# Optimization experiments

Hardware: AMD Instinct MI355X
Metric: run time of the kernel (lower is better)

The kernel has to match this reference:

```python
import jax, jax.numpy as jnp
import numpy as np

N = 100000      # nodes
E = 1600000     # edges
G = 1024        # graphs in batch
NF = 9          # atom features (OGB AtomEncoder)
V = 128         # vocab per atom feature
H = 128         # hidden_dim
L = 3           # num_graph_layers
OUT = 10        # output_dim
BN_EPS = 1e-5


def setup_inputs() -> dict:
    key = jax.random.key(0)
    ks = jax.random.split(key, 12)
    x = jax.random.randint(ks[0], (N, NF), 0, V, dtype=jnp.int32)
    edge_index = jax.random.randint(ks[1], (2, E), 0, N, dtype=jnp.int32)
    batch = jnp.sort(jax.random.randint(ks[2], (N,), 0, G, dtype=jnp.int32))
    emb = jax.random.normal(ks[3], (NF, V, H), dtype=jnp.float32) * 0.05
    Ws = jax.random.normal(ks[4], (L, H, H), dtype=jnp.float32) * (1.0 / np.sqrt(H))
    bs = jnp.zeros((L, H), dtype=jnp.float32)
    gamma = jnp.ones((L - 1, H), dtype=jnp.float32)
    beta = jnp.zeros((L - 1, H), dtype=jnp.float32)
    run_mean = jax.random.normal(ks[5], (L - 1, H), dtype=jnp.float32) * 0.1
    run_var = jax.random.uniform(ks[6], (L - 1, H), minval=0.5, maxval=1.5, dtype=jnp.float32)
    W_clf = jax.random.normal(ks[7], (H, OUT), dtype=jnp.float32) * (1.0 / np.sqrt(H))
    b_clf = jnp.zeros((OUT,), dtype=jnp.float32)
    return {"x": x, "edge_index": edge_index, "batch": batch, "emb": emb,
            "Ws": Ws, "bs": bs, "gamma": gamma, "beta": beta,
            "run_mean": run_mean, "run_var": run_var,
            "W_clf": W_clf, "b_clf": b_clf}


def reference(x, edge_index, batch, emb, Ws, bs, gamma, beta, run_mean, run_var, W_clf, b_clf):
    # Eval-mode forward: dropout = identity, BatchNorm uses running stats.
    src, dst = edge_index[0], edge_index[1]
    # GCN symmetric normalization with self-loops: deg = 1 + in-degree
    deg = jax.ops.segment_sum(jnp.ones((E,), jnp.float32), dst, num_segments=N) + 1.0
    dinv = jax.lax.rsqrt(deg)                 # [N]
    norm_e = dinv[src] * dinv[dst]            # [E] edge coefficient
    norm_self = dinv * dinv                   # [N] self-loop coefficient

    # AtomEncoder: sum of per-feature embedding lookups -> [N, H]
    h = emb[jnp.arange(NF)[None, :], x].sum(axis=1)

    for i in range(L):
        hw = h @ Ws[i]                                                       # [N, H]
        h = (jax.ops.segment_sum(hw[src] * norm_e[:, None], dst, num_segments=N)
             + hw * norm_self[:, None] + bs[i])                              # GCNConv
        if i < L - 1:
            h = (h - run_mean[i]) * (gamma[i] * jax.lax.rsqrt(run_var[i] + BN_EPS)) + beta[i]
            h = jax.nn.relu(h)

    # global mean pool over graphs
    counts = jax.ops.segment_sum(jnp.ones((N,), jnp.float32), batch, num_segments=G)
    pooled = jax.ops.segment_sum(h, batch, num_segments=G) / jnp.maximum(counts, 1.0)[:, None]
    return pooled @ W_clf + b_clf             # [G, OUT]
```

## Files before the change

kernel.cpp:

```cpp
#include <hip/hip_runtime.h>
#include <hip/hip_bf16.h>
#include <hip/hip_fp16.h>

#define NN 100000
#define EE 1600000
#define GG 1024
#define NF 9
#define VV 128
#define HH 128
#define LL 3
#define OUTD 10
#define BN_EPS 1e-5f
#define NBUCK 196
#define BCAP 12288
#define CHUNK 4096
#define NB128 782

typedef __attribute__((ext_vector_type(8))) short short8;
typedef __attribute__((ext_vector_type(4))) float f32x4;

__device__ inline unsigned short f2bf(float x) {
    unsigned u = __float_as_uint(x);
    unsigned r = (u + 0x7fffu + ((u >> 16) & 1u)) >> 16;
    return (unsigned short)r;
}
__device__ inline float bf2f(unsigned short b) { return __uint_as_float(((unsigned)b) << 16); }

__device__ inline void mix8(float a[8], const uint4& r, float nm) {
    asm("v_fma_mix_f32 %0, %8, %12, %0 op_sel:[0,0,0] op_sel_hi:[1,0,0]\n\t"
        "v_fma_mix_f32 %1, %8, %12, %1 op_sel:[1,0,0] op_sel_hi:[1,0,0]\n\t"
        "v_fma_mix_f32 %2, %9, %12, %2 op_sel:[0,0,0] op_sel_hi:[1,0,0]\n\t"
        "v_fma_mix_f32 %3, %9, %12, %3 op_sel:[1,0,0] op_sel_hi:[1,0,0]\n\t"
        "v_fma_mix_f32 %4, %10, %12, %4 op_sel:[0,0,0] op_sel_hi:[1,0,0]\n\t"
        "v_fma_mix_f32 %5, %10, %12, %5 op_sel:[1,0,0] op_sel_hi:[1,0,0]\n\t"
        "v_fma_mix_f32 %6, %11, %12, %6 op_sel:[0,0,0] op_sel_hi:[1,0,0]\n\t"
        "v_fma_mix_f32 %7, %11, %12, %7 op_sel:[1,0,0] op_sel_hi:[1,0,0]"
        : "+v"(a[0]), "+v"(a[1]), "+v"(a[2]), "+v"(a[3]),
          "+v"(a[4]), "+v"(a[5]), "+v"(a[6]), "+v"(a[7])
        : "v"(r.x), "v"(r.y), "v"(r.z), "v"(r.w), "v"(nm));
}

__global__ __launch_bounds__(256) void split_kernel(const int* __restrict__ src,
                                                    const int* __restrict__ dst,
                                                    int* __restrict__ bcur,
                                                    int* __restrict__ bucket_edges) {
    __shared__ int lcnt[256], loff[256], lcur[256], gbase[256], sh[256];
    __shared__ int stage[CHUNK];
    __shared__ unsigned char stageb[CHUNK];
    int tid = threadIdx.x;
    int cs = blockIdx.x * CHUNK;
    int n = min(CHUNK, EE - cs);
    lcnt[tid] = 0;
    __syncthreads();
    for (int i = tid; i < n; i += 256)
        atomicAdd(&lcnt[dst[cs + i] >> 9], 1);
    __syncthreads();
    int val = lcnt[tid];
    sh[tid] = val; __syncthreads();
    for (int d = 1; d < 256; d <<= 1) {
        int t = (tid >= d) ? sh[tid - d] : 0;
        __syncthreads();
        sh[tid] += t;
        __syncthreads();
    }
    loff[tid] = sh[tid] - val;
    lcur[tid] = sh[tid] - val;
    __syncthreads();
    for (int i = tid; i < n; i += 256) {
        int d = dst[cs + i], s = src[cs + i];
        int b = d >> 9;
        int p = atomicAdd(&lcur[b], 1);
        stage[p] = (s << 9) | (d & 511);
        stageb[p] = (unsigned char)b;
    }
    if (val > 0) gbase[tid] = atomicAdd(&bcur[tid], val);
    __syncthreads();
    for (int i = tid; i < n; i += 256) {
        int b = stageb[i];
        bucket_edges[(size_t)b * BCAP + gbase[b] + (i - loff[b])] = stage[i];
    }
}

__global__ __launch_bounds__(256) void bhist_kernel(const int* __restrict__ bcur,
                                                    const int* __restrict__ bucket_edges,
                                                    int* __restrict__ cnt,
                                                    float* __restrict__ dinv,
                                                    int* __restrict__ bsum) {
    __shared__ int lc[512];
    __shared__ int sh[256];
    int b = blockIdx.x, tid = threadIdx.x;
    lc[tid] = 0; lc[tid + 256] = 0;
    __syncthreads();
    int n = bcur[b];
    const int* be = bucket_edges + (size_t)b * BCAP;
    for (int i = tid; i < n; i += 256) atomicAdd(&lc[be[i] & 511], 1);
    __syncthreads();
    int node = b * 512 + tid;
    int c0 = lc[tid], c1 = lc[tid + 256];
    int s = 0;
    if (node < NN) { cnt[node] = c0; dinv[node] = rsqrtf(1.0f + (float)c0); s += c0; }
    if (node + 256 < NN) { cnt[node + 256] = c1; dinv[node + 256] = rsqrtf(1.0f + (float)c1); s += c1; }
    sh[tid] = s; __syncthreads();
    for (int d = 128; d > 0; d >>= 1) { if (tid < d) sh[tid] += sh[tid + d]; __syncthreads(); }
    if (tid == 0) bsum[b] = sh[0];
}

__global__ void scanB_kernel(int* __restrict__ bsum) {
    __shared__ int sh[256];
    int tid = threadIdx.x;
    int v = (tid < NBUCK) ? bsum[tid] : 0;
    sh[tid] = v; __syncthreads();
    for (int d = 1; d < 256; d <<= 1) {
        int t = (tid >= d) ? sh[tid - d] : 0;
        __syncthreads();
        sh[tid] += t;
        __syncthreads();
    }
    if (tid < NBUCK) bsum[tid] = sh[tid] - v;
}

__global__ void scanC_kernel(const int* __restrict__ cnt, const int* __restrict__ bsum,
                             int* __restrict__ row_ptr) {
    __shared__ int sh[256];
    int tid = threadIdx.x;
    int base = blockIdx.x * 512 + tid * 2;
    int v0 = (base < NN) ? cnt[base] : 0;
    int v1 = (base + 1 < NN) ? cnt[base + 1] : 0;
    int ts = v0 + v1;
    sh[tid] = ts; __syncthreads();
    for (int d = 1; d < 256; d <<= 1) {
        int t = (tid >= d) ? sh[tid - d] : 0;
        __syncthreads();
        sh[tid] += t;
        __syncthreads();
    }
    int excl = sh[tid] - ts + bsum[blockIdx.x];
    if (base < NN) row_ptr[base] = excl;
    if (base + 1 < NN) row_ptr[base + 1] = excl + v0;
    if (blockIdx.x == 0 && tid == 0) row_ptr[NN] = EE;
}

__global__ __launch_bounds__(256) void cscatter_kernel(const int* __restrict__ bcur,
                                                       const int* __restrict__ bucket_edges,
                                                       const int* __restrict__ row_ptr,
                                                       const float* __restrict__ dinv,
                                                       int2* __restrict__ col) {
    __shared__ int lcur[512];
    int b = blockIdx.x, tid = threadIdx.x;
    int node0 = b * 512;
#pragma unroll
    for (int k = 0; k < 2; ++k) {
        int j = tid + k * 256;
        int node = node0 + j;
        if (node < NN) lcur[j] = row_ptr[node];
    }
    __syncthreads();
    int n = bcur[b];
    const int* be = bucket_edges + (size_t)b * BCAP;
    for (int i = tid; i < n; i += 256) {
        int w = be[i];
        int j = w & 511;
        int s = (int)((unsigned)w >> 9);
        int p = atomicAdd(&lcur[j], 1);
        float nm = dinv[s] * dinv[node0 + j];
        col[p] = make_int2(s, __float_as_int(nm));
    }
}

__global__ __launch_bounds__(256) void wprep_kernel(const float* __restrict__ Ws,
        const float* __restrict__ Wc, const float* __restrict__ b2,
        unsigned short* __restrict__ WThi, unsigned short* __restrict__ WTlo,
        unsigned short* __restrict__ WcThi, unsigned short* __restrict__ WcTlo,
        float* __restrict__ bb2) {
    int id = blockIdx.x * 256 + threadIdx.x;
    if (id < LL * HH * HH) {
        int layer = id >> 14;
        int rem = id & (HH * HH - 1);
        int k = rem >> 7, n = rem & 127;
        float w = Ws[id];
        unsigned short hi = f2bf(w);
        float lo = w - bf2f(hi);
        WThi[(size_t)layer * HH * HH + n * HH + k] = hi;
        WTlo[(size_t)layer * HH * HH + n * HH + k] = f2bf(lo);
    }
    if (blockIdx.x == 0) {
        int tid = threadIdx.x;
        const float* W2 = Ws + (size_t)2 * HH * HH;
        for (int i = tid; i < 16 * HH; i += 256) {
            int n = i >> 7, k = i & 127;
            float s = 0.f;
            if (n < OUTD) {
                for (int j = 0; j < HH; ++j)
                    s += W2[k * HH + j] * Wc[j * OUTD + n];
            }
            unsigned short hi = f2bf(s);
            WcThi[i] = hi;
            WcTlo[i] = f2bf(s - bf2f(hi));
        }
        if (tid < OUTD) {
            float s = 0.f;
            for (int c = 0; c < HH; ++c) s += b2[c] * Wc[c * OUTD + tid];
            bb2[tid] = s;
        }
    }
}

__global__ __launch_bounds__(256) void enc_mm_kernel(const int* __restrict__ x,
        const float* __restrict__ emb,
        const unsigned short* __restrict__ WThi, const unsigned short* __restrict__ WTlo,
        __half* __restrict__ hw_out) {
    __shared__ __align__(16) unsigned short lh[32][136];
    __shared__ __align__(16) unsigned short ll[32][136];
    int tid = threadIdx.x;
    int nloc = tid >> 3;
    int seg = tid & 7;
    int nodebase = blockIdx.x * 32;
    int n = nodebase + nloc;
    float s[16];
#pragma unroll
    for (int i = 0; i < 16; ++i) s[i] = 0.f;
#pragma unroll
    for (int f = 0; f < NF; ++f) {
        int idx = x[n * NF + f];
        const float4* ep = (const float4*)(emb + ((size_t)(f * VV + idx)) * HH + seg * 16);
#pragma unroll
        for (int q = 0; q < 4; ++q) {
            float4 e = ep[q];
            s[q * 4 + 0] += e.x; s[q * 4 + 1] += e.y;
            s[q * 4 + 2] += e.z; s[q * 4 + 3] += e.w;
        }
    }
#pragma unroll
    for (int q = 0; q < 4; ++q) {
        ushort4 oh, ol;
        oh.x = f2bf(s[q * 4 + 0]); ol.x = f2bf(s[q * 4 + 0] - bf2f(oh.x));
        oh.y = f2bf(s[q * 4 + 1]); ol.y = f2bf(s[q * 4 + 1] - bf2f(oh.y));
        oh.z = f2bf(s[q * 4 + 2]); ol.z = f2bf(s[q * 4 + 2] - bf2f(oh.z));
        oh.w = f2bf(s[q * 4 + 3]); ol.w = f2bf(s[q * 4 + 3] - bf2f(oh.w));
        *(ushort4*)&lh[nloc][seg * 16 + q * 4] = oh;
        *(ushort4*)&ll[nloc][seg * 16 + q * 4] = ol;
    }
    __syncthreads();
    int wave = tid >> 6, lane = tid & 63;
    int quad = lane >> 4, m = lane & 15;
    f32x4 acc[2][2] = {};
    int kq = quad * 8;
#pragma unroll
    for (int t = 0; t < 4; ++t) {
        int k0 = t * 32 + kq;
        short8 a0h = *(const short8*)&lh[m][k0];
        short8 a0l = *(const short8*)&ll[m][k0];
        short8 a1h = *(const short8*)&lh[16 + m][k0];
        short8 a1l = *(const short8*)&ll[16 + m][k0];
#pragma unroll
        for (int c = 0; c < 2; ++c) {
            int ct = wave * 2 + c;
            short8 bh = *(const short8*)(WThi + (size_t)(ct * 16 + m) * HH + k0);
            short8 bl = *(const short8*)(WTlo + (size_t)(ct * 16 + m) * HH + k0);
            acc[0][c] = __builtin_amdgcn_mfma_f32_16x16x32_bf16(a0h, bh, acc[0][c], 0, 0, 0);
            acc[0][c] = __builtin_amdgcn_mfma_f32_16x16x32_bf16(a0l, bh, acc[0][c], 0, 0, 0);
            acc[0][c] = __builtin_amdgcn_mfma_f32_16x16x32_bf16(a0h, bl, acc[0][c], 0, 0, 0);
            acc[1][c] = __builtin_amdgcn_mfma_f32_16x16x32_bf16(a1h, bh, acc[1][c], 0, 0, 0);
            acc[1][c] = __builtin_amdgcn_mfma_f32_16x16x32_bf16(a1l, bh, acc[1][c], 0, 0, 0);
            acc[1][c] = __builtin_amdgcn_mfma_f32_16x16x32_bf16(a1h, bl, acc[1][c], 0, 0, 0);
        }
    }
#pragma unroll
    for (int c = 0; c < 2; ++c) {
        int colx = (wave * 2 + c) * 16 + m;
#pragma unroll
        for (int rt = 0; rt < 2; ++rt) {
            int r0 = nodebase + rt * 16 + quad * 4;
#pragma unroll
            for (int reg = 0; reg < 4; ++reg)
                hw_out[(size_t)(r0 + reg) * HH + colx] = __float2half(acc[rt][c][reg]);
        }
    }
}

__device__ inline void gather_node(const uint4* __restrict__ hw4,
                                   const int2* __restrict__ col,
                                   int start, int end, int c4,
                                   float a[8], float b[8]) {
    int e = start;
    for (; e + 4 <= end; e += 4) {
        unsigned long long w0 = *(const unsigned long long*)&col[e];
        unsigned long long w1 = *(const unsigned long long*)&col[e + 1];
        unsigned long long w2 = *(const unsigned long long*)&col[e + 2];
        unsigned long long w3 = *(const unsigned long long*)&col[e + 3];
        uint4 r0 = hw4[(size_t)(unsigned)(w0 & 0xffffffffu) * 16 + c4];
        uint4 r1 = hw4[(size_t)(unsigned)(w1 & 0xffffffffu) * 16 + c4];
        uint4 r2 = hw4[(size_t)(unsigned)(w2 & 0xffffffffu) * 16 + c4];
        uint4 r3 = hw4[(size_t)(unsigned)(w3 & 0xffffffffu) * 16 + c4];
        mix8(a, r0, __int_as_float((int)(unsigned)(w0 >> 32)));
        mix8(b, r1, __int_as_float((int)(unsigned)(w1 >> 32)));
        mix8(a, r2, __int_as_float((int)(unsigned)(w2 >> 32)));
        mix8(b, r3, __int_as_float((int)(unsigned)(w3 >> 32)));
    }
    if (e < end) {
        int last = end - 1;
        int e1 = min(e + 1, last), e2 = min(e + 2, last), e3 = min(e + 3, last);
        unsigned long long w0 = *(const unsigned long long*)&col[e];
        unsigned long long w1 = *(const unsigned long long*)&col[e1];
        unsigned long long w2 = *(const unsigned long long*)&col[e2];
        unsigned long long w3 = *(const unsigned long long*)&col[e3];
        float n0 = __int_as_float((int)(unsigned)(w0 >> 32));
        float n1 = (e + 1 < end) ? __int_as_float((int)(unsigned)(w1 >> 32)) : 0.f;
        float n2 = (e + 2 < end) ? __int_as_float((int)(unsigned)(w2 >> 32)) : 0.f;
        float n3 = (e + 3 < end) ? __int_as_float((int)(unsigned)(w3 >> 32)) : 0.f;
        uint4 r0 = hw4[(size_t)(unsigned)(w0 & 0xffffffffu) * 16 + c4];
        uint4 r1 = hw4[(size_t)(unsigned)(w1 & 0xffffffffu) * 16 + c4];
        uint4 r2 = hw4[(size_t)(unsigned)(w2 & 0xffffffffu) * 16 + c4];
        uint4 r3 = hw4[(size_t)(unsigned)(w3 & 0xffffffffu) * 16 + c4];
        mix8(a, r0, n0);
        mix8(b, r1, n1);
        mix8(a, r2, n2);
        mix8(b, r3, n3);
    }
}

template<bool DO_PROJ>
__global__ __launch_bounds__(512) void agg_mm_kernel(const __half* __restrict__ hw_in,
    const int* __restrict__ row_ptr, const int2* __restrict__ col,
    const float* __restrict__ dinv,
    const float* __restrict__ bias, const float* __restrict__ gamma,
    const float* __restrict__ beta, const float* __restrict__ rmean,
    const float* __restrict__ rvar,
    const unsigned short* __restrict__ WThi, const unsigned short* __restrict__ WTlo,
    __half* __restrict__ hw_out,
    const unsigned short* __restrict__ WcThi, const unsigned short* __restrict__ WcTlo,
    __half* __restrict__ y_out) {
    __shared__ __align__(16) unsigned short lh[32][136];
    __shared__ __align__(16) unsigned short ll[32][136];
    int wave = threadIdx.x >> 6;
    int lane = threadIdx.x & 63;
    int grp = lane >> 4;
    int c4 = lane & 15;
    int nodebase = blockIdx.x * 32;
    const uint4* hw4 = (const uint4*)hw_in;

    int v = nodebase + wave * 4 + grp;
    int start = row_ptr[v], end = row_ptr[v + 1];
    float a[8] = {}, b[8] = {};
    gather_node(hw4, col, start, end, c4, a, b);

    {
        float dv = dinv[v];
        uint4 r = hw4[(size_t)v * 16 + c4];
        mix8(a, r, dv * dv);
    }
#pragma unroll
    for (int i = 0; i < 8; ++i) a[i] += b[i];

    int ch = c4 * 8;
#pragma unroll
    for (int i = 0; i < 8; ++i) a[i] += bias[ch + i];
#pragma unroll
    for (int i = 0; i < 8; ++i) {
        int c = ch + i;
        float sc = gamma[c] * rsqrtf(rvar[c] + BN_EPS);
        a[i] = fmaxf((a[i] - rmean[c]) * sc + beta[c], 0.f);
    }
    int rloc = wave * 4 + grp;
    ushort4 oh0, oh1, ol0, ol1;
    oh0.x = f2bf(a[0]); ol0.x = f2bf(a[0] - bf2f(oh0.x));
    oh0.y = f2bf(a[1]); ol0.y = f2bf(a[1] - bf2f(oh0.y));
    oh0.z = f2bf(a[2]); ol0.z = f2bf(a[2] - bf2f(oh0.z));
    oh0.w = f2bf(a[3]); ol0.w = f2bf(a[3] - bf2f(oh0.w));
    oh1.x = f2bf(a[4]); ol1.x = f2bf(a[4] - bf2f(oh1.x));
    oh1.y = f2bf(a[5]); ol1.y = f2bf(a[5] - bf2f(oh1.y));
    oh1.z = f2bf(a[6]); ol1.z = f2bf(a[6] - bf2f(oh1.z));
    oh1.w = f2bf(a[7]); ol1.w = f2bf(a[7] - bf2f(oh1.w));
    *(ushort4*)&lh[rloc][ch]     = oh0;
    *(ushort4*)&lh[rloc][ch + 4] = oh1;
    *(ushort4*)&ll[rloc][ch]     = ol0;
    *(ushort4*)&ll[rloc][ch + 4] = ol1;

    __syncthreads();
    int quad = lane >> 4, m = lane & 15;
    f32x4 acc[2] = {};
    int kq = quad * 8;
    int ct = wave;
#pragma unroll
    for (int t = 0; t < 4; ++t) {
        int k0 = t * 32 + kq;
        short8 a0h = *(const short8*)&lh[m][k0];
        short8 a0l = *(const short8*)&ll[m][k0];
        short8 a1h = *(const short8*)&lh[16 + m][k0];
        short8 a1l = *(const short8*)&ll[16 + m][k0];
        short8 bh = *(const short8*)(WThi + (size_t)(ct * 16 + m) * HH + k0);
        short8 bl = *(const short8*)(WTlo + (size_t)(ct * 16 + m) * HH + k0);
        acc[0] = __builtin_amdgcn_mfma_f32_16x16x32_bf16(a0h, bh, acc[0], 0, 0, 0);
        acc[0] = __builtin_amdgcn_mfma_f32_16x16x32_bf16(a0l, bh, acc[0], 0, 0, 0);
        acc[0] = __builtin_amdgcn_mfma_f32_16x16x32_bf16(a0h, bl, acc[0], 0, 0, 0);
        acc[1] = __builtin_amdgcn_mfma_f32_16x16x32_bf16(a1h, bh, acc[1], 0, 0, 0);
        acc[1] = __builtin_amdgcn_mfma_f32_16x16x32_bf16(a1l, bh, acc[1], 0, 0, 0);
        acc[1] = __builtin_amdgcn_mfma_f32_16x16x32_bf16(a1h, bl, acc[1], 0, 0, 0);
    }
    int colx = ct * 16 + m;
#pragma unroll
    for (int rt = 0; rt < 2; ++rt) {
        int r0 = nodebase + rt * 16 + quad * 4;
#pragma unroll
        for (int reg = 0; reg < 4; ++reg)
            hw_out[(size_t)(r0 + reg) * HH + colx] = __float2half(acc[rt][reg]);
    }

    if constexpr (DO_PROJ) {
        if (wave < 2) {
            f32x4 pacc = {};
#pragma unroll
            for (int t = 0; t < 4; ++t) {
                int k0 = t * 32 + kq;
                short8 ah = *(const short8*)&lh[wave * 16 + m][k0];
                short8 al = *(const short8*)&ll[wave * 16 + m][k0];
                short8 bh = *(const short8*)(WcThi + (size_t)m * HH + k0);
                short8 bl = *(const short8*)(WcTlo + (size_t)m * HH + k0);
                pacc = __builtin_amdgcn_mfma_f32_16x16x32_bf16(ah, bh, pacc, 0, 0, 0);
                pacc = __builtin_amdgcn_mfma_f32_16x16x32_bf16(al, bh, pacc, 0, 0, 0);
                pacc = __builtin_amdgcn_mfma_f32_16x16x32_bf16(ah, bl, pacc, 0, 0, 0);
            }
#pragma unroll
            for (int reg = 0; reg < 4; ++reg) {
                int node = nodebase + wave * 16 + quad * 4 + reg;
                y_out[(size_t)node * 16 + m] = __float2half(pacc[reg]);
            }
        }
    }
}

__global__ __launch_bounds__(256) void agg_pool_kernel(const __half* __restrict__ y,
    const int* __restrict__ row_ptr, const int2* __restrict__ col,
    const float* __restrict__ dinv, const int* __restrict__ batch,
    float* __restrict__ pooled) {
    __shared__ __align__(16) float lz[128][16];
    __shared__ int bg[128];
    int tid = threadIdx.x;
    int g2 = tid >> 1;
    int cl = tid & 1;
    int nodebase = blockIdx.x * 128;
    int v = nodebase + g2;
    int vc = min(v, NN - 1);
    int start = row_ptr[vc];
    int end = (v < NN) ? row_ptr[vc + 1] : start;
    const uint4* y4 = (const uint4*)y;
    float a[8] = {};
    int e = start;
    for (; e + 4 <= end; e += 4) {
        unsigned long long w0 = *(const unsigned long long*)&col[e];
        unsigned long long w1 = *(const unsigned long long*)&col[e + 1];
        unsigned long long w2 = *(const unsigned long long*)&col[e + 2];
        unsigned long long w3 = *(const unsigned long long*)&col[e + 3];
        uint4 r0 = y4[(size_t)(unsigned)(w0 & 0xffffffffu) * 2 + cl];
        uint4 r1 = y4[(size_t)(unsigned)(w1 & 0xffffffffu) * 2 + cl];
        uint4 r2 = y4[(size_t)(unsigned)(w2 & 0xffffffffu) * 2 + cl];
        uint4 r3 = y4[(size_t)(unsigned)(w3 & 0xffffffffu) * 2 + cl];
        mix8(a, r0, __int_as_float((int)(unsigned)(w0 >> 32)));
        mix8(a, r1, __int_as_float((int)(unsigned)(w1 >> 32)));
        mix8(a, r2, __int_as_float((int)(unsigned)(w2 >> 32)));
        mix8(a, r3, __int_as_float((int)(unsigned)(w3 >> 32)));
    }
    if (e < end) {
        int last = end - 1;
        int e1 = min(e + 1, last), e2 = min(e + 2, last), e3 = min(e + 3, last);
        unsigned long long w0 = *(const unsigned long long*)&col[e];
        unsigned long long w1 = *(const unsigned long long*)&col[e1];
        unsigned long long w2 = *(const unsigned long long*)&col[e2];
        unsigned long long w3 = *(const unsigned long long*)&col[e3];
        float n0 = __int_as_float((int)(unsigned)(w0 >> 32));
        float n1 = (e + 1 < end) ? __int_as_float((int)(unsigned)(w1 >> 32)) : 0.f;
        float n2 = (e + 2 < end) ? __int_as_float((int)(unsigned)(w2 >> 32)) : 0.f;
        float n3 = (e + 3 < end) ? __int_as_float((int)(unsigned)(w3 >> 32)) : 0.f;
        uint4 r0 = y4[(size_t)(unsigned)(w0 & 0xffffffffu) * 2 + cl];
        uint4 r1 = y4[(size_t)(unsigned)(w1 & 0xffffffffu) * 2 + cl];
        uint4 r2 = y4[(size_t)(unsigned)(w2 & 0xffffffffu) * 2 + cl];
        uint4 r3 = y4[(size_t)(unsigned)(w3 & 0xffffffffu) * 2 + cl];
        mix8(a, r0, n0);
        mix8(a, r1, n1);
        mix8(a, r2, n2);
        mix8(a, r3, n3);
    }
    if (v < NN) {
        float dv = dinv[v];
        uint4 r = y4[(size_t)v * 2 + cl];
        mix8(a, r, dv * dv);
    } else {
#pragma unroll
        for (int i = 0; i < 8; ++i) a[i] = 0.f;
    }
    int chb = cl * 8;
#pragma unroll
    for (int i = 0; i < 8; ++i) lz[g2][chb + i] = a[i];
    if (cl == 0) bg[g2] = batch[vc];
    __syncthreads();
    int ch = tid & 15;
    int rh = tid >> 4;
    int r0i = rh * 8;
    int curg = bg[r0i];
    float run = 0.f;
    for (int r = r0i; r < r0i + 8; ++r) {
        int gg = bg[r];
        if (gg != curg) {
            atomicAdd(&pooled[(size_t)curg * 16 + ch], run);
            run = 0.f; curg = gg;
        }
        run += lz[r][ch];
    }
    atomicAdd(&pooled[(size_t)curg * 16 + ch], run);
}

__global__ __launch_bounds__(256) void finalize_kernel(const float* __restrict__ pooled,
    const int* __restrict__ batch, const float* __restrict__ bb2,
    const float* __restrict__ bc, float* __restrict__ out) {
    int id = blockIdx.x * 256 + threadIdx.x;
    if (id >= GG * 16) return;
    int g = id >> 4, o = id & 15;
    if (o >= OUTD) return;
    int lo = 0, hi = NN;
    while (lo < hi) { int mid = (lo + hi) >> 1; if (batch[mid] < g) lo = mid + 1; else hi = mid; }
    int s0 = lo;
    lo = 0; hi = NN;
    int g1 = g + 1;
    while (lo < hi) { int mid = (lo + hi) >> 1; if (batch[mid] < g1) lo = mid + 1; else hi = mid; }
    int cnt = lo - s0;
    float r = pooled[(size_t)g * 16 + o] / fmaxf((float)cnt, 1.0f);
    out[(size_t)g * OUTD + o] = r + ((cnt > 0) ? bb2[o] : 0.f) + bc[o];
}

extern "C" void kernel_launch(void* const* d_in, const int* in_sizes, int n_in,
                              void* d_out, int out_size, void* d_ws, size_t ws_size,
                              hipStream_t stream) {
    const int*   x      = (const int*)d_in[0];
    const int*   eidx   = (const int*)d_in[1];
    const int*   batch  = (const int*)d_in[2];
    const float* emb    = (const float*)d_in[3];
    const float* Ws     = (const float*)d_in[4];
    const float* bs     = (const float*)d_in[5];
    const float* gamma  = (const float*)d_in[6];
    const float* beta   = (const float*)d_in[7];
    const float* rmean  = (const float*)d_in[8];
    const float* rvar   = (const float*)d_in[9];
    const float* Wclf   = (const float*)d_in[10];
    const float* bclf   = (const float*)d_in[11];
    float* out = (float*)d_out;

    const int* e_src = eidx;
    const int* e_dst = eidx + EE;

    char* ws = (char*)d_ws;
    size_t off = 0;
    auto take = [&](size_t bytes) -> void* {
        void* p = ws + off;
        off = (off + bytes + 255) & ~(size_t)255;
        return p;
    };
    float* dinv     = (float*)take((size_t)NN * 4);
    int*   cnt      = (int*)  take((size_t)NN * 4);
    int*   row_ptr  = (int*)  take((size_t)(NN + 1) * 4);
    int*   bsum     = (int*)  take((size_t)NBUCK * 4);
    int*   bcur     = (int*)  take((size_t)256 * 4);
    int*   bucket_edges = (int*)take((size_t)NBUCK * BCAP * 4);
    int2*  col      = (int2*) take((size_t)EE * 8 + 64);
    __half* hwA     = (__half*)take((size_t)NN * HH * 2);
    __half* hwB     = (__half*)take((size_t)NN * HH * 2);
    __half* yh      = (__half*)take((size_t)NN * 16 * 2);
    float* pooled   = (float*)take((size_t)GG * 16 * 4);
    unsigned short* WThi = (unsigned short*)take((size_t)LL * HH * HH * 2);
    unsigned short* WTlo = (unsigned short*)take((size_t)LL * HH * HH * 2);
    unsigned short* WcThi = (unsigned short*)take((size_t)16 * HH * 2);
    unsigned short* WcTlo = (unsigned short*)take((size_t)16 * HH * 2);
    float* bb2      = (float*)take((size_t)16 * 4);

    hipMemsetAsync(bcur, 0, 256 * 4, stream);
    hipMemsetAsync(pooled, 0, (size_t)GG * 16 * 4, stream);

    split_kernel<<<(EE + CHUNK - 1) / CHUNK, 256, 0, stream>>>(e_src, e_dst, bcur, bucket_edges);
    bhist_kernel<<<NBUCK, 256, 0, stream>>>(bcur, bucket_edges, cnt, dinv, bsum);
    scanB_kernel<<<1, 256, 0, stream>>>(bsum);
    scanC_kernel<<<NBUCK, 256, 0, stream>>>(cnt, bsum, row_ptr);
    cscatter_kernel<<<NBUCK, 256, 0, stream>>>(bcur, bucket_edges, row_ptr, dinv, col);
    wprep_kernel<<<(LL * HH * HH + 255) / 256, 256, 0, stream>>>(Ws, Wclf, bs + 2 * HH,
        WThi, WTlo, WcThi, WcTlo, bb2);

    enc_mm_kernel<<<NN / 32, 256, 0, stream>>>(x, emb, WThi, WTlo, hwA);
    agg_mm_kernel<false><<<NN / 32, 512, 0, stream>>>(hwA, row_ptr, col, dinv,
        bs, gamma, beta, rmean, rvar,
        WThi + (size_t)1 * HH * HH, WTlo + (size_t)1 * HH * HH, hwB,
        nullptr, nullptr, nullptr);
    agg_mm_kernel<true><<<NN / 32, 512, 0, stream>>>(hwB, row_ptr, col, dinv,
        bs + HH, gamma + HH, beta + HH, rmean + HH, rvar + HH,
        WThi + (size_t)2 * HH * HH, WTlo + (size_t)2 * HH * HH, hwA,
        WcThi, WcTlo, yh);
    agg_pool_kernel<<<NB128, 256, 0, stream>>>(yh, row_ptr, col, dinv, batch, pooled);
    finalize_kernel<<<(GG * 16 + 255) / 256, 256, 0, stream>>>(pooled, batch, bb2, bclf, out);
}
```

Before: 411.2 us.

## Replace bucketed CSR build with global-atomic histogram and direct placement

```diff
diff --git a/kernel.cpp b/kernel.cpp
--- a/kernel.cpp
+++ b/kernel.cpp
@@ -11,9 +11,7 @@
 #define LL 3
 #define OUTD 10
 #define BN_EPS 1e-5f
-#define NBUCK 196
-#define BCAP 12288
-#define CHUNK 4096
+#define NB_SCAN 98
 #define NB128 782
 
 typedef __attribute__((ext_vector_type(8))) short short8;
@@ -40,129 +38,75 @@
         : "v"(r.x), "v"(r.y), "v"(r.z), "v"(r.w), "v"(nm));
 }
 
-__global__ __launch_bounds__(256) void split_kernel(const int* __restrict__ src,
-                                                    const int* __restrict__ dst,
-                                                    int* __restrict__ bcur,
-                                                    int* __restrict__ bucket_edges) {
-    __shared__ int lcnt[256], loff[256], lcur[256], gbase[256], sh[256];
-    __shared__ int stage[CHUNK];
-    __shared__ unsigned char stageb[CHUNK];
+__global__ __launch_bounds__(256) void hist_kernel(const int* __restrict__ dst,
+                                                   int* __restrict__ cnt) {
+    int i = blockIdx.x * 256 + threadIdx.x;
+    int stride = gridDim.x * 256;
+    for (; i < EE; i += stride) atomicAdd(&cnt[dst[i]], 1);
+}
+
+__global__ void scanA_kernel(const int* __restrict__ cnt, int* __restrict__ bsum,
+                             float* __restrict__ dinv) {
+    __shared__ int sh[256];
     int tid = threadIdx.x;
-    int cs = blockIdx.x * CHUNK;
-    int n = min(CHUNK, EE - cs);
-    lcnt[tid] = 0;
+    int base = blockIdx.x * 1024 + tid * 4;
+    int s = 0;
+#pragma unroll
+    for (int i = 0; i < 4; ++i) {
+        int idx = base + i;
+        if (idx < NN) {
+            int c = cnt[idx];
+            s += c;
+            dinv[idx] = rsqrtf(1.0f + (float)c);
+        }
+    }
+    sh[tid] = s; __syncthreads();
+    for (int d = 128; d > 0; d >>= 1) { if (tid < d) sh[tid] += sh[tid + d]; __syncthreads(); }
+    if (tid == 0) bsum[blockIdx.x] = sh[0];
+}
+
+__global__ void scanC_kernel(const int* __restrict__ cnt, const int* __restrict__ bsum,
+                             int* __restrict__ row_ptr, int* __restrict__ cur) {
+    __shared__ int sh[256];
+    __shared__ int pre[256];
+    int tid = threadIdx.x;
+    pre[tid] = (tid < blockIdx.x) ? bsum[tid] : 0;
     __syncthreads();
-    for (int i = tid; i < n; i += 256)
-        atomicAdd(&lcnt[dst[cs + i] >> 9], 1);
-    __syncthreads();
-    int val = lcnt[tid];
-    sh[tid] = val; __syncthreads();
+    for (int d = 128; d > 0; d >>= 1) { if (tid < d) pre[tid] += pre[tid + d]; __syncthreads(); }
+    int bbase = pre[0];
+    int base = blockIdx.x * 1024 + tid * 4;
+    int v[4];
+#pragma unroll
+    for (int i = 0; i < 4; ++i) { int idx = base + i; v[i] = (idx < NN) ? cnt[idx] : 0; }
+    int tsum = v[0] + v[1] + v[2] + v[3];
+    sh[tid] = tsum; __syncthreads();
     for (int d = 1; d < 256; d <<= 1) {
         int t = (tid >= d) ? sh[tid - d] : 0;
         __syncthreads();
         sh[tid] += t;
         __syncthreads();
     }
-    loff[tid] = sh[tid] - val;
-    lcur[tid] = sh[tid] - val;
-    __syncthreads();
-    for (int i = tid; i < n; i += 256) {
-        int d = dst[cs + i], s = src[cs + i];
-        int b = d >> 9;
-        int p = atomicAdd(&lcur[b], 1);
-        stage[p] = (s << 9) | (d & 511);
-        stageb[p] = (unsigned char)b;
-    }
-    if (val > 0) gbase[tid] = atomicAdd(&bcur[tid], val);
-    __syncthreads();
-    for (int i = tid; i < n; i += 256) {
-        int b = stageb[i];
-        bucket_edges[(size_t)b * BCAP + gbase[b] + (i - loff[b])] = stage[i];
-    }
-}
-
-__global__ __launch_bounds__(256) void bhist_kernel(const int* __restrict__ bcur,
-                                                    const int* __restrict__ bucket_edges,
-                                                    int* __restrict__ cnt,
-                                                    float* __restrict__ dinv,
-                                                    int* __restrict__ bsum) {
-    __shared__ int lc[512];
-    __shared__ int sh[256];
-    int b = blockIdx.x, tid = threadIdx.x;
-    lc[tid] = 0; lc[tid + 256] = 0;
-    __syncthreads();
-    int n = bcur[b];
-    const int* be = bucket_edges + (size_t)b * BCAP;
-    for (int i = tid; i < n; i += 256) atomicAdd(&lc[be[i] & 511], 1);
-    __syncthreads();
-    int node = b * 512 + tid;
-    int c0 = lc[tid], c1 = lc[tid + 256];
-    int s = 0;
-    if (node < NN) { cnt[node] = c0; dinv[node] = rsqrtf(1.0f + (float)c0); s += c0; }
-    if (node + 256 < NN) { cnt[node + 256] = c1; dinv[node + 256] = rsqrtf(1.0f + (float)c1); s += c1; }
-    sh[tid] = s; __syncthreads();
-    for (int d = 128; d > 0; d >>= 1) { if (tid < d) sh[tid] += sh[tid + d]; __syncthreads(); }
-    if (tid == 0) bsum[b] = sh[0];
-}
-
-__global__ void scanB_kernel(int* __restrict__ bsum) {
-    __shared__ int sh[256];
-    int tid = threadIdx.x;
-    int v = (tid < NBUCK) ? bsum[tid] : 0;
-    sh[tid] = v; __syncthreads();
-    for (int d = 1; d < 256; d <<= 1) {
-        int t = (tid >= d) ? sh[tid - d] : 0;
-        __syncthreads();
-        sh[tid] += t;
-        __syncthreads();
-    }
-    if (tid < NBUCK) bsum[tid] = sh[tid] - v;
-}
-
-__global__ void scanC_kernel(const int* __restrict__ cnt, const int* __restrict__ bsum,
-                             int* __restrict__ row_ptr) {
-    __shared__ int sh[256];
-    int tid = threadIdx.x;
-    int base = blockIdx.x * 512 + tid * 2;
-    int v0 = (base < NN) ? cnt[base] : 0;
-    int v1 = (base + 1 < NN) ? cnt[base + 1] : 0;
-    int ts = v0 + v1;
-    sh[tid] = ts; __syncthreads();
-    for (int d = 1; d < 256; d <<= 1) {
-        int t = (tid >= d) ? sh[tid - d] : 0;
-        __syncthreads();
-        sh[tid] += t;
-        __syncthreads();
-    }
-    int excl = sh[tid] - ts + bsum[blockIdx.x];
-    if (base < NN) row_ptr[base] = excl;
-    if (base + 1 < NN) row_ptr[base + 1] = excl + v0;
+    int excl = sh[tid] - tsum + bbase;
+#pragma unroll
+    for (int i = 0; i < 4; ++i) {
+        int idx = base + i;
+        if (idx < NN) { row_ptr[idx] = excl; cur[idx] = excl; }
+        excl += v[i];
+    }
     if (blockIdx.x == 0 && tid == 0) row_ptr[NN] = EE;
 }
 
-__global__ __launch_bounds__(256) void cscatter_kernel(const int* __restrict__ bcur,
-                                                       const int* __restrict__ bucket_edges,
-                                                       const int* __restrict__ row_ptr,
-                                                       const float* __restrict__ dinv,
-                                                       int2* __restrict__ col) {
-    __shared__ int lcur[512];
-    int b = blockIdx.x, tid = threadIdx.x;
-    int node0 = b * 512;
-#pragma unroll
-    for (int k = 0; k < 2; ++k) {
-        int j = tid + k * 256;
-        int node = node0 + j;
-        if (node < NN) lcur[j] = row_ptr[node];
-    }
-    __syncthreads();
-    int n = bcur[b];
-    const int* be = bucket_edges + (size_t)b * BCAP;
-    for (int i = tid; i < n; i += 256) {
-        int w = be[i];
-        int j = w & 511;
-        int s = (int)((unsigned)w >> 9);
-        int p = atomicAdd(&lcur[j], 1);
-        float nm = dinv[s] * dinv[node0 + j];
+__global__ __launch_bounds__(256) void place_kernel(const int* __restrict__ src,
+                                                    const int* __restrict__ dst,
+                                                    const float* __restrict__ dinv,
+                                                    int* __restrict__ cur,
+                                                    int2* __restrict__ col) {
+    int i = blockIdx.x * 256 + threadIdx.x;
+    int stride = gridDim.x * 256;
+    for (; i < EE; i += stride) {
+        int s = src[i], d = dst[i];
+        int p = atomicAdd(&cur[d], 1);
+        float nm = dinv[s] * dinv[d];
         col[p] = make_int2(s, __float_as_int(nm));
     }
 }
@@ -557,9 +501,8 @@
     float* dinv     = (float*)take((size_t)NN * 4);
     int*   cnt      = (int*)  take((size_t)NN * 4);
     int*   row_ptr  = (int*)  take((size_t)(NN + 1) * 4);
-    int*   bsum     = (int*)  take((size_t)NBUCK * 4);
-    int*   bcur     = (int*)  take((size_t)256 * 4);
-    int*   bucket_edges = (int*)take((size_t)NBUCK * BCAP * 4);
+    int*   cur      = (int*)  take((size_t)NN * 4);
+    int*   bsum     = (int*)  take((size_t)NB_SCAN * 4);
     int2*  col      = (int2*) take((size_t)EE * 8 + 64);
     __half* hwA     = (__half*)take((size_t)NN * HH * 2);
     __half* hwB     = (__half*)take((size_t)NN * HH * 2);
@@ -571,14 +514,13 @@
     unsigned short* WcTlo = (unsigned short*)take((size_t)16 * HH * 2);
     float* bb2      = (float*)take((size_t)16 * 4);
 
-    hipMemsetAsync(bcur, 0, 256 * 4, stream);
+    hipMemsetAsync(cnt, 0, (size_t)NN * 4, stream);
     hipMemsetAsync(pooled, 0, (size_t)GG * 16 * 4, stream);
 
-    split_kernel<<<(EE + CHUNK - 1) / CHUNK, 256, 0, stream>>>(e_src, e_dst, bcur, bucket_edges);
-    bhist_kernel<<<NBUCK, 256, 0, stream>>>(bcur, bucket_edges, cnt, dinv, bsum);
-    scanB_kernel<<<1, 256, 0, stream>>>(bsum);
-    scanC_kernel<<<NBUCK, 256, 0, stream>>>(cnt, bsum, row_ptr);
-    cscatter_kernel<<<NBUCK, 256, 0, stream>>>(bcur, bucket_edges, row_ptr, dinv, col);
+    hist_kernel<<<2048, 256, 0, stream>>>(e_dst, cnt);
+    scanA_kernel<<<NB_SCAN, 256, 0, stream>>>(cnt, bsum, dinv);
+    scanC_kernel<<<NB_SCAN, 256, 0, stream>>>(cnt, bsum, row_ptr, cur);
+    place_kernel<<<2048, 256, 0, stream>>>(e_src, e_dst, dinv, cur, col);
     wprep_kernel<<<(LL * HH * HH + 255) / 256, 256, 0, stream>>>(Ws, Wclf, bs + 2 * HH,
         WThi, WTlo, WcThi, WcTlo, bb2);
 
```

New measurement: 511.4 us. 1.24x slower.

## Fuse edge split with encoder matmul and fold memsets and scanB into neighbours

Applied to the files above, without the earlier changes.

```diff
diff --git a/kernel.cpp b/kernel.cpp
--- a/kernel.cpp
+++ b/kernel.cpp
@@ -14,6 +14,8 @@
 #define NBUCK 196
 #define BCAP 12288
 #define CHUNK 4096
+#define NSPLIT 391
+#define NENC 3125
 #define NB128 782
 
 typedef __attribute__((ext_vector_type(8))) short short8;
@@ -40,44 +42,162 @@
         : "v"(r.x), "v"(r.y), "v"(r.z), "v"(r.w), "v"(nm));
 }
 
-__global__ __launch_bounds__(256) void split_kernel(const int* __restrict__ src,
-                                                    const int* __restrict__ dst,
-                                                    int* __restrict__ bcur,
-                                                    int* __restrict__ bucket_edges) {
-    __shared__ int lcnt[256], loff[256], lcur[256], gbase[256], sh[256];
-    __shared__ int stage[CHUNK];
-    __shared__ unsigned char stageb[CHUNK];
+__global__ __launch_bounds__(256) void wprep_kernel(const float* __restrict__ Ws,
+        const float* __restrict__ Wc, const float* __restrict__ b2,
+        unsigned short* __restrict__ WThi, unsigned short* __restrict__ WTlo,
+        unsigned short* __restrict__ WcThi, unsigned short* __restrict__ WcTlo,
+        float* __restrict__ bb2, int* __restrict__ bcur, float* __restrict__ pooled) {
+    int id = blockIdx.x * 256 + threadIdx.x;
+    if (id < LL * HH * HH) {
+        int layer = id >> 14;
+        int rem = id & (HH * HH - 1);
+        int k = rem >> 7, n = rem & 127;
+        float w = Ws[id];
+        unsigned short hi = f2bf(w);
+        float lo = w - bf2f(hi);
+        WThi[(size_t)layer * HH * HH + n * HH + k] = hi;
+        WTlo[(size_t)layer * HH * HH + n * HH + k] = f2bf(lo);
+    }
     int tid = threadIdx.x;
-    int cs = blockIdx.x * CHUNK;
-    int n = min(CHUNK, EE - cs);
-    lcnt[tid] = 0;
-    __syncthreads();
-    for (int i = tid; i < n; i += 256)
-        atomicAdd(&lcnt[dst[cs + i] >> 9], 1);
-    __syncthreads();
-    int val = lcnt[tid];
-    sh[tid] = val; __syncthreads();
-    for (int d = 1; d < 256; d <<= 1) {
-        int t = (tid >= d) ? sh[tid - d] : 0;
-        __syncthreads();
-        sh[tid] += t;
-        __syncthreads();
-    }
-    loff[tid] = sh[tid] - val;
-    lcur[tid] = sh[tid] - val;
-    __syncthreads();
-    for (int i = tid; i < n; i += 256) {
-        int d = dst[cs + i], s = src[cs + i];
-        int b = d >> 9;
-        int p = atomicAdd(&lcur[b], 1);
-        stage[p] = (s << 9) | (d & 511);
-        stageb[p] = (unsigned char)b;
-    }
-    if (val > 0) gbase[tid] = atomicAdd(&bcur[tid], val);
-    __syncthreads();
-    for (int i = tid; i < n; i += 256) {
-        int b = stageb[i];
-        bucket_edges[(size_t)b * BCAP + gbase[b] + (i - loff[b])] = stage[i];
+    if (blockIdx.x == 0) {
+        const float* W2 = Ws + (size_t)2 * HH * HH;
+        for (int i = tid; i < 16 * HH; i += 256) {
+            int n = i >> 7, k = i & 127;
+            float s = 0.f;
+            if (n < OUTD) {
+                for (int j = 0; j < HH; ++j)
+                    s += W2[k * HH + j] * Wc[j * OUTD + n];
+            }
+            unsigned short hi = f2bf(s);
+            WcThi[i] = hi;
+            WcTlo[i] = f2bf(s - bf2f(hi));
+        }
+        if (tid < OUTD) {
+            float s = 0.f;
+            for (int c = 0; c < HH; ++c) s += b2[c] * Wc[c * OUTD + tid];
+            bb2[tid] = s;
+        }
+    } else if (blockIdx.x == 1) {
+        bcur[tid] = 0;
+    } else if (blockIdx.x >= 2 && blockIdx.x < 66) {
+        pooled[(blockIdx.x - 2) * 256 + tid] = 0.f;
+    }
+}
+
+__global__ __launch_bounds__(256) void split_enc_kernel(
+        const int* __restrict__ src, const int* __restrict__ dst,
+        int* __restrict__ bcur, int* __restrict__ bucket_edges,
+        const int* __restrict__ x, const float* __restrict__ emb,
+        const unsigned short* __restrict__ WThi, const unsigned short* __restrict__ WTlo,
+        __half* __restrict__ hw_out) {
+    __shared__ __align__(16) char smem_raw[25600];
+    int tid = threadIdx.x;
+    if (blockIdx.x < NSPLIT) {
+        int* lcnt  = (int*)smem_raw;
+        int* loff  = lcnt + 256;
+        int* lcur  = loff + 256;
+        int* gbase = lcur + 256;
+        int* sh    = gbase + 256;
+        int* stage = sh + 256;
+        unsigned char* stageb = (unsigned char*)(stage + CHUNK);
+        int cs = blockIdx.x * CHUNK;
+        int n = min(CHUNK, EE - cs);
+        lcnt[tid] = 0;
+        __syncthreads();
+        for (int i = tid; i < n; i += 256)
+            atomicAdd(&lcnt[dst[cs + i] >> 9], 1);
+        __syncthreads();
+        int val = lcnt[tid];
+        sh[tid] = val; __syncthreads();
+        for (int d = 1; d < 256; d <<= 1) {
+            int t = (tid >= d) ? sh[tid - d] : 0;
+            __syncthreads();
+            sh[tid] += t;
+            __syncthreads();
+        }
+        loff[tid] = sh[tid] - val;
+        lcur[tid] = sh[tid] - val;
+        __syncthreads();
+        for (int i = tid; i < n; i += 256) {
+            int d = dst[cs + i], s = src[cs + i];
+            int b = d >> 9;
+            int p = atomicAdd(&lcur[b], 1);
+            stage[p] = (s << 9) | (d & 511);
+            stageb[p] = (unsigned char)b;
+        }
+        if (val > 0) gbase[tid] = atomicAdd(&bcur[tid], val);
+        __syncthreads();
+        for (int i = tid; i < n; i += 256) {
+            int b = stageb[i];
+            bucket_edges[(size_t)b * BCAP + gbase[b] + (i - loff[b])] = stage[i];
+        }
+    } else {
+        unsigned short (*lh)[136] = (unsigned short(*)[136])smem_raw;
+        unsigned short (*ll)[136] = (unsigned short(*)[136])(smem_raw + 32 * 136 * 2);
+        int nloc = tid >> 3;
+        int seg = tid & 7;
+        int nodebase = (blockIdx.x - NSPLIT) * 32;
+        int n = nodebase + nloc;
+        float s[16];
+#pragma unroll
+        for (int i = 0; i < 16; ++i) s[i] = 0.f;
+#pragma unroll
+        for (int f = 0; f < NF; ++f) {
+            int idx = x[n * NF + f];
+            const float4* ep = (const float4*)(emb + ((size_t)(f * VV + idx)) * HH + seg * 16);
+#pragma unroll
+            for (int q = 0; q < 4; ++q) {
+                float4 e = ep[q];
+                s[q * 4 + 0] += e.x; s[q * 4 + 1] += e.y;
+                s[q * 4 + 2] += e.z; s[q * 4 + 3] += e.w;
+            }
+        }
+#pragma unroll
+        for (int q = 0; q < 4; ++q) {
+            ushort4 oh, ol;
+            oh.x = f2bf(s[q * 4 + 0]); ol.x = f2bf(s[q * 4 + 0] - bf2f(oh.x));
+            oh.y = f2bf(s[q * 4 + 1]); ol.y = f2bf(s[q * 4 + 1] - bf2f(oh.y));
+            oh.z = f2bf(s[q * 4 + 2]); ol.z = f2bf(s[q * 4 + 2] - bf2f(oh.z));
+            oh.w = f2bf(s[q * 4 + 3]); ol.w = f2bf(s[q * 4 + 3] - bf2f(oh.w));
+            *(ushort4*)&lh[nloc][seg * 16 + q * 4] = oh;
+            *(ushort4*)&ll[nloc][seg * 16 + q * 4] = ol;
+        }
+        __syncthreads();
+        int wave = tid >> 6, lane = tid & 63;
+        int quad = lane >> 4, m = lane & 15;
+        f32x4 acc[2][2] = {};
+        int kq = quad * 8;
+#pragma unroll
+        for (int t = 0; t < 4; ++t) {
+            int k0 = t * 32 + kq;
+            short8 a0h = *(const short8*)&lh[m][k0];
+            short8 a0l = *(const short8*)&ll[m][k0];
+            short8 a1h = *(const short8*)&lh[16 + m][k0];
+            short8 a1l = *(const short8*)&ll[16 + m][k0];
+#pragma unroll
+            for (int c = 0; c < 2; ++c) {
+                int ct = wave * 2 + c;
+                short8 bh = *(const short8*)(WThi + (size_t)(ct * 16 + m) * HH + k0);
+                short8 bl = *(const short8*)(WTlo + (size_t)(ct * 16 + m) * HH + k0);
+                acc[0][c] = __builtin_amdgcn_mfma_f32_16x16x32_bf16(a0h, bh, acc[0][c], 0, 0, 0);
+                acc[0][c] = __builtin_amdgcn_mfma_f32_16x16x32_bf16(a0l, bh, acc[0][c], 0, 0, 0);
+                acc[0][c] = __builtin_amdgcn_mfma_f32_16x16x32_bf16(a0h, bl, acc[0][c], 0, 0, 0);
+                acc[1][c] = __builtin_amdgcn_mfma_f32_16x16x32_bf16(a1h, bh, acc[1][c], 0, 0, 0);
+                acc[1][c] = __builtin_amdgcn_mfma_f32_16x16x32_bf16(a1l, bh, acc[1][c], 0, 0, 0);
+                acc[1][c] = __builtin_amdgcn_mfma_f32_16x16x32_bf16(a1h, bl, acc[1][c], 0, 0, 0);
+            }
+        }
+#pragma unroll
+        for (int c = 0; c < 2; ++c) {
+            int colx = (wave * 2 + c) * 16 + m;
+#pragma unroll
+            for (int rt = 0; rt < 2; ++rt) {
+                int r0 = nodebase + rt * 16 + quad * 4;
+#pragma unroll
+                for (int reg = 0; reg < 4; ++reg)
+                    hw_out[(size_t)(r0 + reg) * HH + colx] = __float2half(acc[rt][c][reg]);
+            }
+        }
     }
 }
 
@@ -105,24 +225,15 @@
     if (tid == 0) bsum[b] = sh[0];
 }
 
-__global__ void scanB_kernel(int* __restrict__ bsum) {
-    __shared__ int sh[256];
-    int tid = threadIdx.x;
-    int v = (tid < NBUCK) ? bsum[tid] : 0;
-    sh[tid] = v; __syncthreads();
-    for (int d = 1; d < 256; d <<= 1) {
-        int t = (tid >= d) ? sh[tid - d] : 0;
-        __syncthreads();
-        sh[tid] += t;
-        __syncthreads();
-    }
-    if (tid < NBUCK) bsum[tid] = sh[tid] - v;
-}
-
 __global__ void scanC_kernel(const int* __restrict__ cnt, const int* __restrict__ bsum,
                              int* __restrict__ row_ptr) {
     __shared__ int sh[256];
+    __shared__ int pre[256];
     int tid = threadIdx.x;
+    pre[tid] = (tid < blockIdx.x && tid < NBUCK) ? bsum[tid] : 0;
+    __syncthreads();
+    for (int d = 128; d > 0; d >>= 1) { if (tid < d) pre[tid] += pre[tid + d]; __syncthreads(); }
+    int bbase = pre[0];
     int base = blockIdx.x * 512 + tid * 2;
     int v0 = (base < NN) ? cnt[base] : 0;
     int v1 = (base + 1 < NN) ? cnt[base + 1] : 0;
@@ -134,7 +245,7 @@
         sh[tid] += t;
         __syncthreads();
     }
-    int excl = sh[tid] - ts + bsum[blockIdx.x];
+    int excl = sh[tid] - ts + bbase;
     if (base < NN) row_ptr[base] = excl;
     if (base + 1 < NN) row_ptr[base + 1] = excl + v0;
     if (blockIdx.x == 0 && tid == 0) row_ptr[NN] = EE;
@@ -164,117 +275,6 @@
         int p = atomicAdd(&lcur[j], 1);
         float nm = dinv[s] * dinv[node0 + j];
         col[p] = make_int2(s, __float_as_int(nm));
-    }
-}
-
-__global__ __launch_bounds__(256) void wprep_kernel(const float* __restrict__ Ws,
-        const float* __restrict__ Wc, const float* __restrict__ b2,
-        unsigned short* __restrict__ WThi, unsigned short* __restrict__ WTlo,
-        unsigned short* __restrict__ WcThi, unsigned short* __restrict__ WcTlo,
-        float* __restrict__ bb2) {
-    int id = blockIdx.x * 256 + threadIdx.x;
-    if (id < LL * HH * HH) {
-        int layer = id >> 14;
-        int rem = id & (HH * HH - 1);
-        int k = rem >> 7, n = rem & 127;
-        float w = Ws[id];
-        unsigned short hi = f2bf(w);
-        float lo = w - bf2f(hi);
-        WThi[(size_t)layer * HH * HH + n * HH + k] = hi;
-        WTlo[(size_t)layer * HH * HH + n * HH + k] = f2bf(lo);
-    }
-    if (blockIdx.x == 0) {
-        int tid = threadIdx.x;
-        const float* W2 = Ws + (size_t)2 * HH * HH;
-        for (int i = tid; i < 16 * HH; i += 256) {
-            int n = i >> 7, k = i & 127;
-            float s = 0.f;
-            if (n < OUTD) {
-                for (int j = 0; j < HH; ++j)
-                    s += W2[k * HH + j] * Wc[j * OUTD + n];
-            }
-            unsigned short hi = f2bf(s);
-            WcThi[i] = hi;
-            WcTlo[i] = f2bf(s - bf2f(hi));
-        }
-        if (tid < OUTD) {
-            float s = 0.f;
-            for (int c = 0; c < HH; ++c) s += b2[c] * Wc[c * OUTD + tid];
-            bb2[tid] = s;
-        }
-    }
-}
-
-__global__ __launch_bounds__(256) void enc_mm_kernel(const int* __restrict__ x,
-        const float* __restrict__ emb,
-        const unsigned short* __restrict__ WThi, const unsigned short* __restrict__ WTlo,
-        __half* __restrict__ hw_out) {
-    __shared__ __align__(16) unsigned short lh[32][136];
-    __shared__ __align__(16) unsigned short ll[32][136];
-    int tid = threadIdx.x;
-    int nloc = tid >> 3;
-    int seg = tid & 7;
-    int nodebase = blockIdx.x * 32;
-    int n = nodebase + nloc;
-    float s[16];
-#pragma unroll
-    for (int i = 0; i < 16; ++i) s[i] = 0.f;
-#pragma unroll
-    for (int f = 0; f < NF; ++f) {
-        int idx = x[n * NF + f];
-        const float4* ep = (const float4*)(emb + ((size_t)(f * VV + idx)) * HH + seg * 16);
-#pragma unroll
-        for (int q = 0; q < 4; ++q) {
-            float4 e = ep[q];
-            s[q * 4 + 0] += e.x; s[q * 4 + 1] += e.y;
-            s[q * 4 + 2] += e.z; s[q * 4 + 3] += e.w;
-        }
-    }
-#pragma unroll
-    for (int q = 0; q < 4; ++q) {
-        ushort4 oh, ol;
-        oh.x = f2bf(s[q * 4 + 0]); ol.x = f2bf(s[q * 4 + 0] - bf2f(oh.x));
-        oh.y = f2bf(s[q * 4 + 1]); ol.y = f2bf(s[q * 4 + 1] - bf2f(oh.y));
-        oh.z = f2bf(s[q * 4 + 2]); ol.z = f2bf(s[q * 4 + 2] - bf2f(oh.z));
-        oh.w = f2bf(s[q * 4 + 3]); ol.w = f2bf(s[q * 4 + 3] - bf2f(oh.w));
-        *(ushort4*)&lh[nloc][seg * 16 + q * 4] = oh;
-        *(ushort4*)&ll[nloc][seg * 16 + q * 4] = ol;
-    }
-    __syncthreads();
-    int wave = tid >> 6, lane = tid & 63;
-    int quad = lane >> 4, m = lane & 15;
-    f32x4 acc[2][2] = {};
-    int kq = quad * 8;
-#pragma unroll
-    for (int t = 0; t < 4; ++t) {
-        int k0 = t * 32 + kq;
-        short8 a0h = *(const short8*)&lh[m][k0];
-        short8 a0l = *(const short8*)&ll[m][k0];
-        short8 a1h = *(const short8*)&lh[16 + m][k0];
-        short8 a1l = *(const short8*)&ll[16 + m][k0];
-#pragma unroll
-        for (int c = 0; c < 2; ++c) {
-            int ct = wave * 2 + c;
-            short8 bh = *(const short8*)(WThi + (size_t)(ct * 16 + m) * HH + k0);
-            short8 bl = *(const short8*)(WTlo + (size_t)(ct * 16 + m) * HH + k0);
-            acc[0][c] = __builtin_amdgcn_mfma_f32_16x16x32_bf16(a0h, bh, acc[0][c], 0, 0, 0);
-            acc[0][c] = __builtin_amdgcn_mfma_f32_16x16x32_bf16(a0l, bh, acc[0][c], 0, 0, 0);
-            acc[0][c] = __builtin_amdgcn_mfma_f32_16x16x32_bf16(a0h, bl, acc[0][c], 0, 0, 0);
-            acc[1][c] = __builtin_amdgcn_mfma_f32_16x16x32_bf16(a1h, bh, acc[1][c], 0, 0, 0);
-            acc[1][c] = __builtin_amdgcn_mfma_f32_16x16x32_bf16(a1l, bh, acc[1][c], 0, 0, 0);
-            acc[1][c] = __builtin_amdgcn_mfma_f32_16x16x32_bf16(a1h, bl, acc[1][c], 0, 0, 0);
-        }
-    }
-#pragma unroll
-    for (int c = 0; c < 2; ++c) {
-        int colx = (wave * 2 + c) * 16 + m;
-#pragma unroll
-        for (int rt = 0; rt < 2; ++rt) {
-            int r0 = nodebase + rt * 16 + quad * 4;
-#pragma unroll
-            for (int reg = 0; reg < 4; ++reg)
-                hw_out[(size_t)(r0 + reg) * HH + colx] = __float2half(acc[rt][c][reg]);
-        }
     }
 }
 
@@ -571,18 +571,14 @@
     unsigned short* WcTlo = (unsigned short*)take((size_t)16 * HH * 2);
     float* bb2      = (float*)take((size_t)16 * 4);
 
-    hipMemsetAsync(bcur, 0, 256 * 4, stream);
-    hipMemsetAsync(pooled, 0, (size_t)GG * 16 * 4, stream);
-
-    split_kernel<<<(EE + CHUNK - 1) / CHUNK, 256, 0, stream>>>(e_src, e_dst, bcur, bucket_edges);
+    wprep_kernel<<<(LL * HH * HH + 255) / 256, 256, 0, stream>>>(Ws, Wclf, bs + 2 * HH,
+        WThi, WTlo, WcThi, WcTlo, bb2, bcur, pooled);
+    split_enc_kernel<<<NSPLIT + NENC, 256, 0, stream>>>(e_src, e_dst, bcur, bucket_edges,
+        x, emb, WThi, WTlo, hwA);
     bhist_kernel<<<NBUCK, 256, 0, stream>>>(bcur, bucket_edges, cnt, dinv, bsum);
-    scanB_kernel<<<1, 256, 0, stream>>>(bsum);
     scanC_kernel<<<NBUCK, 256, 0, stream>>>(cnt, bsum, row_ptr);
     cscatter_kernel<<<NBUCK, 256, 0, stream>>>(bcur, bucket_edges, row_ptr, dinv, col);
-    wprep_kernel<<<(LL * HH * HH + 255) / 256, 256, 0, stream>>>(Ws, Wclf, bs + 2 * HH,
-        WThi, WTlo, WcThi, WcTlo, bb2);
-
-    enc_mm_kernel<<<NN / 32, 256, 0, stream>>>(x, emb, WThi, WTlo, hwA);
+
     agg_mm_kernel<false><<<NN / 32, 512, 0, stream>>>(hwA, row_ptr, col, dinv,
         bs, gamma, beta, rmean, rvar,
         WThi + (size_t)1 * HH * HH, WTlo + (size_t)1 * HH * HH, hwB,
```

New measurement: 394.7 us. 4.0% less time.
